# Kernel tuning notes

Hardware: AMD Instinct MI355X
Metric: run time of the kernel (lower is better)

The kernel has to match this reference:

```python
import jax, jax.numpy as jnp
import numpy as np

D_MODEL = 512
EXPAND = 2
D_INNER = D_MODEL * EXPAND  # 1024
D_STATE = 64
D_CONV = 4
DT_BASE = 0.1
MAX_STEPS = 10
THRESH = 1e-4
DAMPING = 0.5
B_SZ, L = 1, 256


def setup_inputs() -> dict:
    key = jax.random.key(0)
    ks = jax.random.split(key, 12)
    rn = lambda k, shape, s=0.02: jax.random.normal(k, shape, jnp.float32) * s
    x = jax.random.normal(ks[0], (B_SZ, L, D_MODEL), jnp.float32)
    # in_proj: Linear(d_model -> 2*d_inner, bias=False); stored (in, out)
    W_in = rn(ks[1], (D_MODEL, 2 * D_INNER))
    # depthwise causal conv1d, kernel (d_inner, 1, d_conv) + bias
    conv_w = rn(ks[2], (D_INNER, 1, D_CONV), 0.2)
    conv_b = rn(ks[3], (D_INNER,), 0.02)
    # SSM kernel params (A_log initialized exactly as in the module)
    A_log = jnp.log(jnp.broadcast_to(jnp.arange(1, D_STATE + 1, dtype=jnp.float32), (D_INNER, D_STATE)))
    W_B = rn(ks[4], (D_INNER, D_STATE))
    W_C = rn(ks[5], (D_INNER, D_STATE))
    D = jnp.ones((D_INNER,), jnp.float32)
    dt_w1 = rn(ks[6], (D_INNER, D_INNER // 4))
    dt_b1 = jnp.zeros((D_INNER // 4,), jnp.float32)
    dt_w2 = rn(ks[7], (D_INNER // 4, D_INNER))
    dt_b2 = jnp.zeros((D_INNER,), jnp.float32)
    W_out = rn(ks[8], (D_INNER, D_MODEL))
    ln_in_g = jnp.ones((D_MODEL,), jnp.float32)
    ln_in_b = jnp.zeros((D_MODEL,), jnp.float32)
    ln_out_g = jnp.ones((D_MODEL,), jnp.float32)
    ln_out_b = jnp.zeros((D_MODEL,), jnp.float32)
    return dict(x=x, W_in=W_in, conv_w=conv_w, conv_b=conv_b, A_log=A_log, W_B=W_B, W_C=W_C, D=D,
                dt_w1=dt_w1, dt_b1=dt_b1, dt_w2=dt_w2, dt_b2=dt_b2, W_out=W_out,
                ln_in_g=ln_in_g, ln_in_b=ln_in_b, ln_out_g=ln_out_g, ln_out_b=ln_out_b)


def _ln(x, g, b, eps=1e-5):
    m = jnp.mean(x, axis=-1, keepdims=True)
    v = jnp.mean((x - m) ** 2, axis=-1, keepdims=True)
    return (x - m) / jnp.sqrt(v + eps) * g + b


def _forward(x, W_in, conv_w, conv_b, A_log, W_B, W_C, D, dt_w1, dt_b1, dt_w2, dt_b2, W_out,
             ln_in_g, ln_in_b, ln_out_g, ln_out_b):
    residual = x
    xn = _ln(x, ln_in_g, ln_in_b)
    xz = xn @ W_in                                  # (b, l, 2*d_inner)
    x_inner, z = jnp.split(xz, 2, axis=-1)
    # depthwise causal conv (pad d_conv-1 on the left == pad both sides then take [:L])
    xc = jnp.transpose(x_inner, (0, 2, 1))          # (b, d, l)
    xc = jax.lax.conv_general_dilated(xc, conv_w, window_strides=(1,),
                                      padding=[(D_CONV - 1, 0)],
                                      feature_group_count=D_INNER)
    xc = xc + conv_b[None, :, None]
    x_inner = jax.nn.silu(jnp.transpose(xc, (0, 2, 1)))  # (b, l, d_inner)

    # --- kernel quantities (loop-invariant: depend only on x_inner) ---
    A = -jnp.exp(A_log)                             # (d, n)
    Bm = x_inner @ W_B                              # (b, l, n)
    Cm = x_inner @ W_C                              # (b, l, n)
    dt = jax.nn.gelu(x_inner @ dt_w1 + dt_b1, approximate=False) @ dt_w2 + dt_b2
    dt = jax.nn.softplus(dt) * DT_BASE              # (b, l, d)
    A_bar = jnp.exp(jnp.einsum('bld,dn->bldn', dt, A))          # (b, l, d, n)
    Bx = (dt * x_inner)[..., None] * Bm[:, :, None, :]           # B_bar * x, (b, l, d, n)

    # --- fixed-point evolution with convergence-gated freeze (== early break) ---
    h = jnp.zeros_like(A_bar)
    y_h = h  # h_new that produces the output y
    converged = jnp.array(False)
    h_diff = jnp.float32(0.0)
    for _ in range(MAX_STEPS):
        h_new = A_bar * h + Bx
        dh = h_new - h
        diff = jnp.mean(jnp.sqrt(jnp.sum(dh * dh, axis=(-2, -1))))  # mean Frobenius norm over (b,l)
        y_h = jnp.where(converged, y_h, h_new)
        h_diff = jnp.where(converged, h_diff, diff)
        converged = converged | (diff < THRESH)
        # damping update skipped after break (converged)
        h = jnp.where(converged, h, DAMPING * h_new + (1.0 - DAMPING) * h)

    y = jnp.einsum('bldn,bln->bld', y_h, Cm) + D * x_inner
    y = y * jax.nn.silu(z)
    out = _ln(y @ W_out, ln_out_g, ln_out_b) + residual
    return out


def reference(x, W_in, conv_w, conv_b, A_log, W_B, W_C, D, dt_w1, dt_b1, dt_w2, dt_b2, W_out,
              ln_in_g, ln_in_b, ln_out_g, ln_out_b):
    return _forward(x, W_in, conv_w, conv_b, A_log, W_B, W_C, D, dt_w1, dt_b1, dt_w2, dt_b2,
                    W_out, ln_in_g, ln_in_b, ln_out_g, ln_out_b)
```

## Files before the change

kernel.cpp:

```cpp
#include <hip/hip_runtime.h>
#include <cmath>

#define L 256
#define DMODEL 512
#define DINNER 1024
#define DSTATE 64
#define NSTEPS 10
#define TK 32

template <int NS>
__global__ __launch_bounds__(256) void ln_kernel(
    const float* __restrict__ in, int islice, const float* __restrict__ g,
    const float* __restrict__ b, const float* __restrict__ resid,
    float* __restrict__ out) {
  const int l = blockIdx.x, tid = threadIdx.x;
  float x0 = 0.0f, x1 = 0.0f;
#pragma unroll
  for (int s = 0; s < NS; ++s) {
    x0 += in[s * islice + l * DMODEL + tid];
    x1 += in[s * islice + l * DMODEL + tid + 256];
  }
  float sm = x0 + x1, q = x0 * x0 + x1 * x1;
#pragma unroll
  for (int off = 32; off; off >>= 1) {
    sm += __shfl_down(sm, off);
    q += __shfl_down(q, off);
  }
  __shared__ float sw[4], qw[4];
  __shared__ float mS, rS;
  if ((tid & 63) == 0) { sw[tid >> 6] = sm; qw[tid >> 6] = q; }
  __syncthreads();
  if (tid == 0) {
    float S = sw[0] + sw[1] + sw[2] + sw[3];
    float Q = qw[0] + qw[1] + qw[2] + qw[3];
    float m = S * (1.0f / DMODEL);
    float v = Q * (1.0f / DMODEL) - m * m;
    mS = m;
    rS = rsqrtf(v + 1e-5f);
  }
  __syncthreads();
  const float m = mS, r = rS;
  float o0 = (x0 - m) * r * g[tid] + b[tid];
  float o1 = (x1 - m) * r * g[tid + 256] + b[tid + 256];
  if (resid) {
    o0 += resid[l * DMODEL + tid];
    o1 += resid[l * DMODEL + tid + 256];
  }
  out[l * DMODEL + tid] = o0;
  out[l * DMODEL + tid + 256] = o1;
}

template <int MODE>
__global__ __launch_bounds__(256) void gemm32(
    const float* __restrict__ A, int lda, int aslice,
    const float* __restrict__ B, int ldb, float* __restrict__ C, int ldc,
    int cslice, int kchunk, const float* __restrict__ abias,
    const float* __restrict__ WB, const float* __restrict__ WC,
    const float* __restrict__ W1) {
  __shared__ float As[TK][33];
  __shared__ float Bs[TK][64];
  const int tid = threadIdx.x;
  const int tx = tid & 15, ty = tid >> 4;
  const int m0 = blockIdx.y * 32, n0 = blockIdx.x * 64;
  const int k0 = blockIdx.z * kchunk;
  const float* Bp = B;
  int ld = ldb, nb = n0;
  if (MODE == 1) {
    if (n0 < 64) { Bp = WB; ld = 64; nb = n0; }
    else if (n0 < 128) { Bp = WC; ld = 64; nb = n0 - 64; }
    else { Bp = W1; ld = 256; nb = n0 - 128; }
  }
  const int ar = tid >> 3, ac = (tid & 7) * 4;
  const int br = tid >> 4, bc = (tid & 15) * 4;
  float acc[2][4] = {};
  for (int kk0 = 0; kk0 < kchunk; kk0 += TK) {
    const int kb = k0 + kk0;
    float v[4];
    if (MODE == 2) {
      v[0] = v[1] = v[2] = v[3] = 0.0f;
#pragma unroll
      for (int s = 0; s < 4; ++s) {
        const float4 t =
            *(const float4*)&A[s * aslice + (m0 + ar) * lda + kb + ac];
        v[0] += t.x; v[1] += t.y; v[2] += t.z; v[3] += t.w;
      }
#pragma unroll
      for (int j = 0; j < 4; ++j) {
        const float x = v[j] + abias[kb + ac + j];
        v[j] = 0.5f * x * (1.0f + erff(x * 0.70710678118654752f));
      }
    } else {
      const float4 t = *(const float4*)&A[(m0 + ar) * lda + kb + ac];
      v[0] = t.x; v[1] = t.y; v[2] = t.z; v[3] = t.w;
    }
#pragma unroll
    for (int j = 0; j < 4; ++j) As[ac + j][ar] = v[j];
#pragma unroll
    for (int i = 0; i < 2; ++i)
      *(float4*)&Bs[br + i * 16][bc] =
          *(const float4*)&Bp[(kb + br + i * 16) * ld + nb + bc];
    __syncthreads();
#pragma unroll
    for (int kk = 0; kk < TK; ++kk) {
      const float a0 = As[kk][ty * 2], a1 = As[kk][ty * 2 + 1];
      const float4 bv = *(const float4*)&Bs[kk][tx * 4];
      const float* bp = (const float*)&bv;
#pragma unroll
      for (int j = 0; j < 4; ++j) {
        acc[0][j] = fmaf(a0, bp[j], acc[0][j]);
        acc[1][j] = fmaf(a1, bp[j], acc[1][j]);
      }
    }
    __syncthreads();
  }
  float* Cp = C + (size_t)blockIdx.z * cslice;
#pragma unroll
  for (int i = 0; i < 2; ++i)
    *(float4*)&Cp[(m0 + ty * 2 + i) * ldc + n0 + tx * 4] = *(float4*)&acc[i][0];
}

__global__ __launch_bounds__(256) void conv_silu_kernel(
    const float* __restrict__ xz, const float* __restrict__ cw,
    const float* __restrict__ cb, float* __restrict__ xi) {
  const int d = blockIdx.x * 256 + threadIdx.x;
  const int l = blockIdx.y;
  const float4 w = *(const float4*)&cw[d * 4];
  const float* wp = (const float*)&w;
  float s = cb[d];
#pragma unroll
  for (int j = 0; j < 4; ++j) {
    const int ll = l - 3 + j;
    if (ll >= 0) s = fmaf(wp[j], xz[ll * (2 * DINNER) + d], s);
  }
  xi[l * DINNER + d] = s / (1.0f + expf(-s));
}

__global__ __launch_bounds__(256) void pass1_kernel(
    const float* __restrict__ dtbp, const float* __restrict__ dt_b2,
    const float* __restrict__ xi, const float* __restrict__ bctp,
    float* __restrict__ accLp) {
  const int l = blockIdx.y, tid = threadIdx.x;
  const int d = blockIdx.x * 256 + tid;
  __shared__ float B2[DSTATE];
  if (tid < DSTATE) {
    float b = 0.0f;
#pragma unroll
    for (int s = 0; s < 4; ++s) b += bctp[s * 98304 + l * 384 + tid];
    B2[tid] = b * b;
  }
  __syncthreads();
  const float dr =
      dtbp[l * DINNER + d] + dtbp[262144 + l * DINNER + d] + dt_b2[d];
  const float sp = (dr > 20.0f) ? dr : log1pf(expf(dr));
  const float dtv = 0.1f * sp;
  const float xv = xi[l * DINNER + d];
  float w0 = dtv * xv;
  w0 *= w0;
  const float q = expf(-dtv);
  float acc[NSTEPS] = {};
  float a = 1.0f;
  for (int n = 0; n < DSTATE; ++n) {
    a *= q;
    const float r = fmaf(0.5f, a, 0.5f);
    const float s2 = r * r;
    float p = w0 * B2[n];
#pragma unroll
    for (int k = 0; k < NSTEPS; ++k) {
      acc[k] += p;
      p *= s2;
    }
  }
  __shared__ float sred[4][NSTEPS];
#pragma unroll
  for (int k = 0; k < NSTEPS; ++k) {
    float v = acc[k];
#pragma unroll
    for (int off = 32; off; off >>= 1) v += __shfl_down(v, off);
    if ((tid & 63) == 0) sred[tid >> 6][k] = v;
  }
  __syncthreads();
  if (tid < NSTEPS)
    accLp[blockIdx.x * (L * NSTEPS) + l * NSTEPS + tid] =
        sred[0][tid] + sred[1][tid] + sred[2][tid] + sred[3][tid];
}

__global__ __launch_bounds__(256) void pass2_kernel(
    const float* __restrict__ dtbp, const float* __restrict__ dt_b2,
    const float* __restrict__ xi, const float* __restrict__ bctp,
    const float* __restrict__ xz, const float* __restrict__ Dv,
    const float* __restrict__ accLp, float* __restrict__ y) {
  const int l = blockIdx.y, tid = threadIdx.x;
  const int d = blockIdx.x * 256 + tid;
  __shared__ float sred[4];
  __shared__ float diffs[NSTEPS];
  __shared__ int Ksh;
#pragma unroll
  for (int k = 0; k < NSTEPS; ++k) {
    float v = accLp[tid * NSTEPS + k] + accLp[2560 + tid * NSTEPS + k] +
              accLp[5120 + tid * NSTEPS + k] + accLp[7680 + tid * NSTEPS + k];
    v = sqrtf(v);
#pragma unroll
    for (int off = 32; off; off >>= 1) v += __shfl_down(v, off);
    if ((tid & 63) == 0) sred[tid >> 6] = v;
    __syncthreads();
    if (tid == 0)
      diffs[k] = (sred[0] + sred[1] + sred[2] + sred[3]) * (1.0f / L);
    __syncthreads();
  }
  __shared__ float P[DSTATE];
  if (tid == 0) {
    int K = NSTEPS;
    for (int k = 0; k < NSTEPS; ++k) {
      if (diffs[k] < 1e-4f) { K = k + 1; break; }
    }
    Ksh = K;
  }
  if (tid < DSTATE) {
    float bm = 0.0f, cm = 0.0f;
#pragma unroll
    for (int s = 0; s < 4; ++s) {
      bm += bctp[s * 98304 + l * 384 + tid];
      cm += bctp[s * 98304 + l * 384 + 64 + tid];
    }
    P[tid] = bm * cm;
  }
  __syncthreads();
  const int K = Ksh;
  const float dr =
      dtbp[l * DINNER + d] + dtbp[262144 + l * DINNER + d] + dt_b2[d];
  const float sp = (dr > 20.0f) ? dr : log1pf(expf(dr));
  const float dtv = 0.1f * sp;
  const float xv = xi[l * DINNER + d];
  const float dtx = dtv * xv;
  const float q = expf(-dtv);
  float a = 1.0f, s = 0.0f;
  for (int n = 0; n < DSTATE; ++n) {
    a *= q;
    const float r = fmaf(0.5f, a, 0.5f);
    float c = 0.0f;
    for (int k = 1; k < K; ++k) c = fmaf(r, c, 0.5f);
    const float hn = fmaf(a, c, 1.0f);
    s = fmaf(hn, P[n], s);
  }
  float yv = fmaf(dtx, s, Dv[d] * xv);
  const float zv = xz[l * (2 * DINNER) + DINNER + d];
  yv *= zv / (1.0f + expf(-zv));
  y[l * DINNER + d] = yv;
}

extern "C" void kernel_launch(void* const* d_in, const int* in_sizes, int n_in,
                              void* d_out, int out_size, void* d_ws,
                              size_t ws_size, hipStream_t stream) {
  const float* x = (const float*)d_in[0];
  const float* W_in = (const float*)d_in[1];
  const float* conv_w = (const float*)d_in[2];
  const float* conv_b = (const float*)d_in[3];
  const float* W_B = (const float*)d_in[5];
  const float* W_C = (const float*)d_in[6];
  const float* Dv = (const float*)d_in[7];
  const float* dt_w1 = (const float*)d_in[8];
  const float* dt_b1 = (const float*)d_in[9];
  const float* dt_w2 = (const float*)d_in[10];
  const float* dt_b2 = (const float*)d_in[11];
  const float* W_out = (const float*)d_in[12];
  const float* ln_in_g = (const float*)d_in[13];
  const float* ln_in_b = (const float*)d_in[14];
  const float* ln_out_g = (const float*)d_in[15];
  const float* ln_out_b = (const float*)d_in[16];
  float* out = (float*)d_out;

  float* ws = (float*)d_ws;
  float* xn = ws;
  float* xz = xn + 131072;
  float* xi = xz + 524288;
  float* bctp = xi + 262144;
  float* dtbp = bctp + 393216;
  float* accLp = dtbp + 524288;
  float* yop = accLp + 10240;

  ln_kernel<1><<<L, 256, 0, stream>>>(x, 0, ln_in_g, ln_in_b, nullptr, xn);
  gemm32<0><<<dim3(32, 8, 1), 256, 0, stream>>>(
      xn, DMODEL, 0, W_in, 2 * DINNER, xz, 2 * DINNER, 0, DMODEL, nullptr,
      nullptr, nullptr, nullptr);
  conv_silu_kernel<<<dim3(4, L), 256, 0, stream>>>(xz, conv_w, conv_b, xi);
  gemm32<1><<<dim3(6, 8, 4), 256, 0, stream>>>(
      xi, DINNER, 0, nullptr, 0, bctp, 384, 98304, 256, nullptr, W_B, W_C,
      dt_w1);
  gemm32<2><<<dim3(16, 8, 2), 256, 0, stream>>>(
      bctp + 128, 384, 98304, dt_w2, DINNER, dtbp, DINNER, 262144, 128, dt_b1,
      nullptr, nullptr, nullptr);
  pass1_kernel<<<dim3(4, L), 256, 0, stream>>>(dtbp, dt_b2, xi, bctp, accLp);
  pass2_kernel<<<dim3(4, L), 256, 0, stream>>>(dtbp, dt_b2, xi, bctp, xz, Dv,
                                               accLp, xi);
  gemm32<0><<<dim3(8, 8, 4), 256, 0, stream>>>(
      xi, DINNER, 0, W_out, DMODEL, yop, DMODEL, 131072, 256, nullptr, nullptr,
      nullptr, nullptr);
  ln_kernel<4><<<L, 256, 0, stream>>>(yop, 131072, ln_out_g, ln_out_b, x, out);
}
```

Baseline: 192.3 us.

## Fuse all stages into one cooperative persistent kernel with grid syncs

Replaces the nine separate kernel launches with a single cooperative kernel of 512 blocks that runs each stage in turn, separated by grid-wide barriers. Work splits are changed so every stage uses about 512 blocks: more split-K partials, two channels per thread in the elementwise passes, and a separate single-block K-selection stage. The goal is to remove launch gaps and tail effects between many small stages. In exchange it adds grid-sync cost, writes more partial buffers that readers must sum, and keeps a multi-launch fallback if the cooperative launch fails.

```diff
diff --git a/kernel.cpp b/kernel.cpp
--- a/kernel.cpp
+++ b/kernel.cpp
@@ -1,45 +1,70 @@
 #include <hip/hip_runtime.h>
+#include <hip/hip_cooperative_groups.h>
 #include <cmath>
+
+namespace cg = cooperative_groups;
 
 #define L 256
 #define DMODEL 512
 #define DINNER 1024
 #define DSTATE 64
 #define NSTEPS 10
-#define TK 32
+
+struct Args {
+  const float *x, *W_in, *conv_w, *conv_b, *W_B, *W_C, *Dv;
+  const float *dt_w1, *dt_b1, *dt_w2, *dt_b2, *W_out;
+  const float *ln_in_g, *ln_in_b, *ln_out_g, *ln_out_b;
+  float* out;
+  float *xn, *xz, *xi, *bctp, *dtbp, *accLp, *yop;
+  int* Kp;
+};
+
+struct SMem {
+  float As[32][34];
+  float Bs[32][64];
+  float red[4][NSTEPS];
+  float vec[DSTATE];
+  float diffs[NSTEPS];
+  float mS, rS;
+};
+
+__device__ __forceinline__ float gelu_f(float x) {
+  return 0.5f * x * (1.0f + erff(x * 0.70710678118654752f));
+}
 
 template <int NS>
-__global__ __launch_bounds__(256) void ln_kernel(
-    const float* __restrict__ in, int islice, const float* __restrict__ g,
-    const float* __restrict__ b, const float* __restrict__ resid,
-    float* __restrict__ out) {
-  const int l = blockIdx.x, tid = threadIdx.x;
+__device__ void stage_ln(SMem& sm, const float* in, int islice, const float* g,
+                         const float* b, const float* resid, float* out,
+                         int gid, int tid) {
+  if (gid >= 256) return;
+  const int l = gid;
   float x0 = 0.0f, x1 = 0.0f;
 #pragma unroll
   for (int s = 0; s < NS; ++s) {
     x0 += in[s * islice + l * DMODEL + tid];
     x1 += in[s * islice + l * DMODEL + tid + 256];
   }
-  float sm = x0 + x1, q = x0 * x0 + x1 * x1;
+  float sv = x0 + x1, q = x0 * x0 + x1 * x1;
 #pragma unroll
   for (int off = 32; off; off >>= 1) {
-    sm += __shfl_down(sm, off);
+    sv += __shfl_down(sv, off);
     q += __shfl_down(q, off);
   }
-  __shared__ float sw[4], qw[4];
-  __shared__ float mS, rS;
-  if ((tid & 63) == 0) { sw[tid >> 6] = sm; qw[tid >> 6] = q; }
+  if ((tid & 63) == 0) {
+    sm.red[tid >> 6][0] = sv;
+    sm.red[tid >> 6][1] = q;
+  }
   __syncthreads();
   if (tid == 0) {
-    float S = sw[0] + sw[1] + sw[2] + sw[3];
-    float Q = qw[0] + qw[1] + qw[2] + qw[3];
+    float S = sm.red[0][0] + sm.red[1][0] + sm.red[2][0] + sm.red[3][0];
+    float Q = sm.red[0][1] + sm.red[1][1] + sm.red[2][1] + sm.red[3][1];
     float m = S * (1.0f / DMODEL);
     float v = Q * (1.0f / DMODEL) - m * m;
-    mS = m;
-    rS = rsqrtf(v + 1e-5f);
-  }
-  __syncthreads();
-  const float m = mS, r = rS;
+    sm.mS = m;
+    sm.rS = rsqrtf(v + 1e-5f);
+  }
+  __syncthreads();
+  const float m = sm.mS, r = sm.rS;
   float o0 = (x0 - m) * r * g[tid] + b[tid];
   float o1 = (x1 - m) * r * g[tid + 256] + b[tid + 256];
   if (resid) {
@@ -50,250 +75,321 @@
   out[l * DMODEL + tid + 256] = o1;
 }
 
-template <int MODE>
-__global__ __launch_bounds__(256) void gemm32(
-    const float* __restrict__ A, int lda, int aslice,
-    const float* __restrict__ B, int ldb, float* __restrict__ C, int ldc,
-    int cslice, int kchunk, const float* __restrict__ abias,
-    const float* __restrict__ WB, const float* __restrict__ WC,
-    const float* __restrict__ W1) {
-  __shared__ float As[TK][33];
-  __shared__ float Bs[TK][64];
-  const int tid = threadIdx.x;
-  const int tx = tid & 15, ty = tid >> 4;
-  const int m0 = blockIdx.y * 32, n0 = blockIdx.x * 64;
-  const int k0 = blockIdx.z * kchunk;
-  const float* Bp = B;
-  int ld = ldb, nb = n0;
-  if (MODE == 1) {
-    if (n0 < 64) { Bp = WB; ld = 64; nb = n0; }
-    else if (n0 < 128) { Bp = WC; ld = 64; nb = n0 - 64; }
-    else { Bp = W1; ld = 256; nb = n0 - 128; }
-  }
-  const int ar = tid >> 3, ac = (tid & 7) * 4;
+__device__ void gemm_tile(SMem& sm, const float* A, int lda, int aslice,
+                          int nslA, const float* abias, const float* B, int ldb,
+                          int nb, float* C, int ldc, int nc, int m0, int kbase,
+                          int ktiles, int tid) {
+  const int rowg = tid >> 4, colg = tid & 15;
+  float acc0[4] = {}, acc1[4] = {};
+  const int ar = tid >> 3, ka = (tid & 7) * 4;
   const int br = tid >> 4, bc = (tid & 15) * 4;
-  float acc[2][4] = {};
-  for (int kk0 = 0; kk0 < kchunk; kk0 += TK) {
-    const int kb = k0 + kk0;
-    float v[4];
-    if (MODE == 2) {
-      v[0] = v[1] = v[2] = v[3] = 0.0f;
-#pragma unroll
-      for (int s = 0; s < 4; ++s) {
-        const float4 t =
-            *(const float4*)&A[s * aslice + (m0 + ar) * lda + kb + ac];
-        v[0] += t.x; v[1] += t.y; v[2] += t.z; v[3] += t.w;
+  for (int t = 0; t < ktiles; ++t) {
+    const int kb = kbase + t * 32;
+    {
+      const float* ap = &A[(size_t)(m0 + ar) * lda + kb + ka];
+      float v[4];
+      if (nslA == 1) {
+        const float4 t4 = *(const float4*)ap;
+        v[0] = t4.x; v[1] = t4.y; v[2] = t4.z; v[3] = t4.w;
+      } else {
+        v[0] = v[1] = v[2] = v[3] = 0.0f;
+        for (int s = 0; s < nslA; ++s) {
+          const float4 t4 = *(const float4*)&ap[(size_t)s * aslice];
+          v[0] += t4.x; v[1] += t4.y; v[2] += t4.z; v[3] += t4.w;
+        }
       }
+      if (abias) {
+#pragma unroll
+        for (int j = 0; j < 4; ++j) v[j] = gelu_f(v[j] + abias[kb + ka + j]);
+      }
+#pragma unroll
+      for (int j = 0; j < 4; ++j) sm.As[ka + j][ar] = v[j];
+    }
+#pragma unroll
+    for (int i = 0; i < 2; ++i)
+      *(float4*)&sm.Bs[br + 16 * i][bc] =
+          *(const float4*)&B[(size_t)(kb + br + 16 * i) * ldb + nb + bc];
+    __syncthreads();
+#pragma unroll
+    for (int kk = 0; kk < 32; ++kk) {
+      const float2 av = *(const float2*)&sm.As[kk][rowg * 2];
+      const float4 bv = *(const float4*)&sm.Bs[kk][colg * 4];
+      const float* bp = (const float*)&bv;
 #pragma unroll
       for (int j = 0; j < 4; ++j) {
-        const float x = v[j] + abias[kb + ac + j];
-        v[j] = 0.5f * x * (1.0f + erff(x * 0.70710678118654752f));
+        acc0[j] = fmaf(av.x, bp[j], acc0[j]);
+        acc1[j] = fmaf(av.y, bp[j], acc1[j]);
       }
-    } else {
-      const float4 t = *(const float4*)&A[(m0 + ar) * lda + kb + ac];
-      v[0] = t.x; v[1] = t.y; v[2] = t.z; v[3] = t.w;
-    }
-#pragma unroll
-    for (int j = 0; j < 4; ++j) As[ac + j][ar] = v[j];
-#pragma unroll
-    for (int i = 0; i < 2; ++i)
-      *(float4*)&Bs[br + i * 16][bc] =
-          *(const float4*)&Bp[(kb + br + i * 16) * ld + nb + bc];
+    }
     __syncthreads();
-#pragma unroll
-    for (int kk = 0; kk < TK; ++kk) {
-      const float a0 = As[kk][ty * 2], a1 = As[kk][ty * 2 + 1];
-      const float4 bv = *(const float4*)&Bs[kk][tx * 4];
-      const float* bp = (const float*)&bv;
-#pragma unroll
-      for (int j = 0; j < 4; ++j) {
-        acc[0][j] = fmaf(a0, bp[j], acc[0][j]);
-        acc[1][j] = fmaf(a1, bp[j], acc[1][j]);
-      }
-    }
-    __syncthreads();
-  }
-  float* Cp = C + (size_t)blockIdx.z * cslice;
-#pragma unroll
-  for (int i = 0; i < 2; ++i)
-    *(float4*)&Cp[(m0 + ty * 2 + i) * ldc + n0 + tx * 4] = *(float4*)&acc[i][0];
-}
-
-__global__ __launch_bounds__(256) void conv_silu_kernel(
-    const float* __restrict__ xz, const float* __restrict__ cw,
-    const float* __restrict__ cb, float* __restrict__ xi) {
-  const int d = blockIdx.x * 256 + threadIdx.x;
-  const int l = blockIdx.y;
-  const float4 w = *(const float4*)&cw[d * 4];
-  const float* wp = (const float*)&w;
-  float s = cb[d];
-#pragma unroll
-  for (int j = 0; j < 4; ++j) {
-    const int ll = l - 3 + j;
-    if (ll >= 0) s = fmaf(wp[j], xz[ll * (2 * DINNER) + d], s);
-  }
-  xi[l * DINNER + d] = s / (1.0f + expf(-s));
-}
-
-__global__ __launch_bounds__(256) void pass1_kernel(
-    const float* __restrict__ dtbp, const float* __restrict__ dt_b2,
-    const float* __restrict__ xi, const float* __restrict__ bctp,
-    float* __restrict__ accLp) {
-  const int l = blockIdx.y, tid = threadIdx.x;
-  const int d = blockIdx.x * 256 + tid;
-  __shared__ float B2[DSTATE];
+  }
+  *(float4*)&C[(size_t)(m0 + rowg * 2) * ldc + nc + colg * 4] =
+      *(float4*)&acc0[0];
+  *(float4*)&C[(size_t)(m0 + rowg * 2 + 1) * ldc + nc + colg * 4] =
+      *(float4*)&acc1[0];
+}
+
+__device__ void stage_inproj(const Args& a, SMem& sm, int gid, int tid) {
+  if (gid >= 512) return;
+  const int kz = gid >> 8, rem = gid & 255;
+  const int mt = rem >> 5, nt = rem & 31;
+  gemm_tile(sm, a.xn, DMODEL, 0, 1, nullptr, a.W_in, 2048, nt * 64,
+            a.xz + kz * 524288, 2048, nt * 64, mt * 32, kz * 256, 8, tid);
+}
+
+__device__ void stage_conv(const Args& a, int gid, int tid) {
+  if (gid >= 512) return;
+  const int l = gid >> 1;
+#pragma unroll
+  for (int dd = 0; dd < 2; ++dd) {
+    const int d = (gid & 1) * 512 + dd * 256 + tid;
+    const float4 w = *(const float4*)&a.conv_w[d * 4];
+    const float* wp = (const float*)&w;
+    float s = a.conv_b[d];
+#pragma unroll
+    for (int j = 0; j < 4; ++j) {
+      const int ll = l - 3 + j;
+      if (ll >= 0)
+        s = fmaf(wp[j], a.xz[ll * 2048 + d] + a.xz[524288 + ll * 2048 + d], s);
+    }
+    a.xi[l * DINNER + d] = s / (1.0f + expf(-s));
+  }
+}
+
+__device__ void stage_bct(const Args& a, SMem& sm, int gid, int tid) {
+  if (gid >= 384) return;
+  const int kz = gid / 48, rem = gid % 48;
+  const int mt = rem / 6, nt = rem % 6;
+  const float* Bp;
+  int ldb, nb;
+  if (nt == 0) { Bp = a.W_B; ldb = 64; nb = 0; }
+  else if (nt == 1) { Bp = a.W_C; ldb = 64; nb = 0; }
+  else { Bp = a.dt_w1; ldb = 256; nb = (nt - 2) * 64; }
+  gemm_tile(sm, a.xi, DINNER, 0, 1, nullptr, Bp, ldb, nb, a.bctp + kz * 98304,
+            384, nt * 64, mt * 32, kz * 128, 4, tid);
+}
+
+__device__ void stage_dt2(const Args& a, SMem& sm, int gid, int tid) {
+  if (gid >= 512) return;
+  const int kz = gid >> 7, rem = gid & 127;
+  const int mt = rem >> 4, nt = rem & 15;
+  gemm_tile(sm, a.bctp + 128, 384, 98304, 8, a.dt_b1, a.dt_w2, 1024, nt * 64,
+            a.dtbp + kz * 262144, 1024, nt * 64, mt * 32, kz * 64, 2, tid);
+}
+
+__device__ void stage_pass1(const Args& a, SMem& sm, int gid, int tid) {
+  if (gid >= 512) return;
+  const int l = gid >> 1, bx = gid & 1;
   if (tid < DSTATE) {
     float b = 0.0f;
 #pragma unroll
-    for (int s = 0; s < 4; ++s) b += bctp[s * 98304 + l * 384 + tid];
-    B2[tid] = b * b;
-  }
-  __syncthreads();
-  const float dr =
-      dtbp[l * DINNER + d] + dtbp[262144 + l * DINNER + d] + dt_b2[d];
-  const float sp = (dr > 20.0f) ? dr : log1pf(expf(dr));
-  const float dtv = 0.1f * sp;
-  const float xv = xi[l * DINNER + d];
-  float w0 = dtv * xv;
-  w0 *= w0;
-  const float q = expf(-dtv);
+    for (int s = 0; s < 8; ++s) b += a.bctp[s * 98304 + l * 384 + tid];
+    sm.vec[tid] = b * b;
+  }
+  __syncthreads();
   float acc[NSTEPS] = {};
-  float a = 1.0f;
-  for (int n = 0; n < DSTATE; ++n) {
-    a *= q;
-    const float r = fmaf(0.5f, a, 0.5f);
-    const float s2 = r * r;
-    float p = w0 * B2[n];
-#pragma unroll
-    for (int k = 0; k < NSTEPS; ++k) {
-      acc[k] += p;
-      p *= s2;
-    }
-  }
-  __shared__ float sred[4][NSTEPS];
+#pragma unroll
+  for (int dd = 0; dd < 2; ++dd) {
+    const int d = bx * 512 + dd * 256 + tid;
+    float dr = a.dt_b2[d];
+#pragma unroll
+    for (int s = 0; s < 4; ++s) dr += a.dtbp[s * 262144 + l * DINNER + d];
+    const float sp = (dr > 20.0f) ? dr : log1pf(expf(dr));
+    const float dtv = 0.1f * sp;
+    const float xv = a.xi[l * DINNER + d];
+    float w0 = dtv * xv;
+    w0 *= w0;
+    const float q = expf(-dtv);
+    float aa = 1.0f;
+    for (int n = 0; n < DSTATE; ++n) {
+      aa *= q;
+      const float r = fmaf(0.5f, aa, 0.5f);
+      const float s2 = r * r;
+      float p = w0 * sm.vec[n];
+#pragma unroll
+      for (int k = 0; k < NSTEPS; ++k) {
+        acc[k] += p;
+        p *= s2;
+      }
+    }
+  }
 #pragma unroll
   for (int k = 0; k < NSTEPS; ++k) {
     float v = acc[k];
 #pragma unroll
     for (int off = 32; off; off >>= 1) v += __shfl_down(v, off);
-    if ((tid & 63) == 0) sred[tid >> 6][k] = v;
+    if ((tid & 63) == 0) sm.red[tid >> 6][k] = v;
   }
   __syncthreads();
   if (tid < NSTEPS)
-    accLp[blockIdx.x * (L * NSTEPS) + l * NSTEPS + tid] =
-        sred[0][tid] + sred[1][tid] + sred[2][tid] + sred[3][tid];
-}
-
-__global__ __launch_bounds__(256) void pass2_kernel(
-    const float* __restrict__ dtbp, const float* __restrict__ dt_b2,
-    const float* __restrict__ xi, const float* __restrict__ bctp,
-    const float* __restrict__ xz, const float* __restrict__ Dv,
-    const float* __restrict__ accLp, float* __restrict__ y) {
-  const int l = blockIdx.y, tid = threadIdx.x;
-  const int d = blockIdx.x * 256 + tid;
-  __shared__ float sred[4];
-  __shared__ float diffs[NSTEPS];
-  __shared__ int Ksh;
+    a.accLp[bx * 2560 + l * NSTEPS + tid] =
+        sm.red[0][tid] + sm.red[1][tid] + sm.red[2][tid] + sm.red[3][tid];
+}
+
+__device__ void stage_kselect(const Args& a, SMem& sm, int gid, int tid) {
+  if (gid != 0) return;
 #pragma unroll
   for (int k = 0; k < NSTEPS; ++k) {
-    float v = accLp[tid * NSTEPS + k] + accLp[2560 + tid * NSTEPS + k] +
-              accLp[5120 + tid * NSTEPS + k] + accLp[7680 + tid * NSTEPS + k];
+    float v = a.accLp[tid * NSTEPS + k] + a.accLp[2560 + tid * NSTEPS + k];
     v = sqrtf(v);
 #pragma unroll
     for (int off = 32; off; off >>= 1) v += __shfl_down(v, off);
-    if ((tid & 63) == 0) sred[tid >> 6] = v;
+    if ((tid & 63) == 0) sm.red[tid >> 6][0] = v;
     __syncthreads();
     if (tid == 0)
-      diffs[k] = (sred[0] + sred[1] + sred[2] + sred[3]) * (1.0f / L);
+      sm.diffs[k] = (sm.red[0][0] + sm.red[1][0] + sm.red[2][0] + sm.red[3][0]) *
+                    (1.0f / L);
     __syncthreads();
   }
-  __shared__ float P[DSTATE];
   if (tid == 0) {
     int K = NSTEPS;
     for (int k = 0; k < NSTEPS; ++k) {
-      if (diffs[k] < 1e-4f) { K = k + 1; break; }
-    }
-    Ksh = K;
-  }
+      if (sm.diffs[k] < 1e-4f) { K = k + 1; break; }
+    }
+    a.Kp[0] = K;
+  }
+}
+
+__device__ void stage_pass2(const Args& a, SMem& sm, int gid, int tid) {
+  if (gid >= 512) return;
+  const int l = gid >> 1, bx = gid & 1;
   if (tid < DSTATE) {
     float bm = 0.0f, cm = 0.0f;
 #pragma unroll
-    for (int s = 0; s < 4; ++s) {
-      bm += bctp[s * 98304 + l * 384 + tid];
-      cm += bctp[s * 98304 + l * 384 + 64 + tid];
-    }
-    P[tid] = bm * cm;
-  }
-  __syncthreads();
-  const int K = Ksh;
-  const float dr =
-      dtbp[l * DINNER + d] + dtbp[262144 + l * DINNER + d] + dt_b2[d];
-  const float sp = (dr > 20.0f) ? dr : log1pf(expf(dr));
-  const float dtv = 0.1f * sp;
-  const float xv = xi[l * DINNER + d];
-  const float dtx = dtv * xv;
-  const float q = expf(-dtv);
-  float a = 1.0f, s = 0.0f;
-  for (int n = 0; n < DSTATE; ++n) {
-    a *= q;
-    const float r = fmaf(0.5f, a, 0.5f);
-    float c = 0.0f;
-    for (int k = 1; k < K; ++k) c = fmaf(r, c, 0.5f);
-    const float hn = fmaf(a, c, 1.0f);
-    s = fmaf(hn, P[n], s);
-  }
-  float yv = fmaf(dtx, s, Dv[d] * xv);
-  const float zv = xz[l * (2 * DINNER) + DINNER + d];
-  yv *= zv / (1.0f + expf(-zv));
-  y[l * DINNER + d] = yv;
+    for (int s = 0; s < 8; ++s) {
+      bm += a.bctp[s * 98304 + l * 384 + tid];
+      cm += a.bctp[s * 98304 + l * 384 + 64 + tid];
+    }
+    sm.vec[tid] = bm * cm;
+  }
+  __syncthreads();
+  const int K = a.Kp[0];
+#pragma unroll
+  for (int dd = 0; dd < 2; ++dd) {
+    const int d = bx * 512 + dd * 256 + tid;
+    float dr = a.dt_b2[d];
+#pragma unroll
+    for (int s = 0; s < 4; ++s) dr += a.dtbp[s * 262144 + l * DINNER + d];
+    const float sp = (dr > 20.0f) ? dr : log1pf(expf(dr));
+    const float dtv = 0.1f * sp;
+    const float xv = a.xi[l * DINNER + d];
+    const float dtx = dtv * xv;
+    const float q = expf(-dtv);
+    float aa = 1.0f, s = 0.0f;
+    for (int n = 0; n < DSTATE; ++n) {
+      aa *= q;
+      const float r = fmaf(0.5f, aa, 0.5f);
+      float c = 0.0f;
+      for (int k = 1; k < K; ++k) c = fmaf(r, c, 0.5f);
+      const float hn = fmaf(aa, c, 1.0f);
+      s = fmaf(hn, sm.vec[n], s);
+    }
+    float yv = fmaf(dtx, s, a.Dv[d] * xv);
+    const float zv =
+        a.xz[l * 2048 + 1024 + d] + a.xz[524288 + l * 2048 + 1024 + d];
+    yv *= zv / (1.0f + expf(-zv));
+    a.xi[l * DINNER + d] = yv;
+  }
+}
+
+__device__ void stage_outproj(const Args& a, SMem& sm, int gid, int tid) {
+  if (gid >= 512) return;
+  const int kz = gid >> 6, rem = gid & 63;
+  const int mt = rem >> 3, nt = rem & 7;
+  gemm_tile(sm, a.xi, DINNER, 0, 1, nullptr, a.W_out, DMODEL, nt * 64,
+            a.yop + kz * 131072, DMODEL, nt * 64, mt * 32, kz * 128, 4, tid);
+}
+
+__global__ __launch_bounds__(256, 2) void fused_kernel(Args a) {
+  __shared__ SMem sm;
+  cg::grid_group grid = cg::this_grid();
+  const int gid = blockIdx.x, tid = threadIdx.x;
+  stage_ln<1>(sm, a.x, 0, a.ln_in_g, a.ln_in_b, nullptr, a.xn, gid, tid);
+  grid.sync();
+  stage_inproj(a, sm, gid, tid);
+  grid.sync();
+  stage_conv(a, gid, tid);
+  grid.sync();
+  stage_bct(a, sm, gid, tid);
+  grid.sync();
+  stage_dt2(a, sm, gid, tid);
+  grid.sync();
+  stage_pass1(a, sm, gid, tid);
+  grid.sync();
+  stage_kselect(a, sm, gid, tid);
+  grid.sync();
+  stage_pass2(a, sm, gid, tid);
+  grid.sync();
+  stage_outproj(a, sm, gid, tid);
+  grid.sync();
+  stage_ln<8>(sm, a.yop, 131072, a.ln_out_g, a.ln_out_b, a.x, a.out, gid, tid);
+}
+
+template <int S>
+__global__ __launch_bounds__(256, 2) void stage_kernel(Args a) {
+  __shared__ SMem sm;
+  const int gid = blockIdx.x, tid = threadIdx.x;
+  if constexpr (S == 0)
+    stage_ln<1>(sm, a.x, 0, a.ln_in_g, a.ln_in_b, nullptr, a.xn, gid, tid);
+  else if constexpr (S == 1) stage_inproj(a, sm, gid, tid);
+  else if constexpr (S == 2) stage_conv(a, gid, tid);
+  else if constexpr (S == 3) stage_bct(a, sm, gid, tid);
+  else if constexpr (S == 4) stage_dt2(a, sm, gid, tid);
+  else if constexpr (S == 5) stage_pass1(a, sm, gid, tid);
+  else if constexpr (S == 6) stage_kselect(a, sm, gid, tid);
+  else if constexpr (S == 7) stage_pass2(a, sm, gid, tid);
+  else if constexpr (S == 8) stage_outproj(a, sm, gid, tid);
+  else if constexpr (S == 9)
+    stage_ln<8>(sm, a.yop, 131072, a.ln_out_g, a.ln_out_b, a.x, a.out, gid,
+                tid);
 }
 
 extern "C" void kernel_launch(void* const* d_in, const int* in_sizes, int n_in,
                               void* d_out, int out_size, void* d_ws,
                               size_t ws_size, hipStream_t stream) {
-  const float* x = (const float*)d_in[0];
-  const float* W_in = (const float*)d_in[1];
-  const float* conv_w = (const float*)d_in[2];
-  const float* conv_b = (const float*)d_in[3];
-  const float* W_B = (const float*)d_in[5];
-  const float* W_C = (const float*)d_in[6];
-  const float* Dv = (const float*)d_in[7];
-  const float* dt_w1 = (const float*)d_in[8];
-  const float* dt_b1 = (const float*)d_in[9];
-  const float* dt_w2 = (const float*)d_in[10];
-  const float* dt_b2 = (const float*)d_in[11];
-  const float* W_out = (const float*)d_in[12];
-  const float* ln_in_g = (const float*)d_in[13];
-  const float* ln_in_b = (const float*)d_in[14];
-  const float* ln_out_g = (const float*)d_in[15];
-  const float* ln_out_b = (const float*)d_in[16];
-  float* out = (float*)d_out;
+  Args a;
+  a.x = (const float*)d_in[0];
+  a.W_in = (const float*)d_in[1];
+  a.conv_w = (const float*)d_in[2];
+  a.conv_b = (const float*)d_in[3];
+  a.W_B = (const float*)d_in[5];
+  a.W_C = (const float*)d_in[6];
+  a.Dv = (const float*)d_in[7];
+  a.dt_w1 = (const float*)d_in[8];
+  a.dt_b1 = (const float*)d_in[9];
+  a.dt_w2 = (const float*)d_in[10];
+  a.dt_b2 = (const float*)d_in[11];
+  a.W_out = (const float*)d_in[12];
+  a.ln_in_g = (const float*)d_in[13];
+  a.ln_in_b = (const float*)d_in[14];
+  a.ln_out_g = (const float*)d_in[15];
+  a.ln_out_b = (const float*)d_in[16];
+  a.out = (float*)d_out;
 
   float* ws = (float*)d_ws;
-  float* xn = ws;
-  float* xz = xn + 131072;
-  float* xi = xz + 524288;
-  float* bctp = xi + 262144;
-  float* dtbp = bctp + 393216;
-  float* accLp = dtbp + 524288;
-  float* yop = accLp + 10240;
-
-  ln_kernel<1><<<L, 256, 0, stream>>>(x, 0, ln_in_g, ln_in_b, nullptr, xn);
-  gemm32<0><<<dim3(32, 8, 1), 256, 0, stream>>>(
-      xn, DMODEL, 0, W_in, 2 * DINNER, xz, 2 * DINNER, 0, DMODEL, nullptr,
-      nullptr, nullptr, nullptr);
-  conv_silu_kernel<<<dim3(4, L), 256, 0, stream>>>(xz, conv_w, conv_b, xi);
-  gemm32<1><<<dim3(6, 8, 4), 256, 0, stream>>>(
-      xi, DINNER, 0, nullptr, 0, bctp, 384, 98304, 256, nullptr, W_B, W_C,
-      dt_w1);
-  gemm32<2><<<dim3(16, 8, 2), 256, 0, stream>>>(
-      bctp + 128, 384, 98304, dt_w2, DINNER, dtbp, DINNER, 262144, 128, dt_b1,
-      nullptr, nullptr, nullptr);
-  pass1_kernel<<<dim3(4, L), 256, 0, stream>>>(dtbp, dt_b2, xi, bctp, accLp);
-  pass2_kernel<<<dim3(4, L), 256, 0, stream>>>(dtbp, dt_b2, xi, bctp, xz, Dv,
-                                               accLp, xi);
-  gemm32<0><<<dim3(8, 8, 4), 256, 0, stream>>>(
-      xi, DINNER, 0, W_out, DMODEL, yop, DMODEL, 131072, 256, nullptr, nullptr,
-      nullptr, nullptr);
-  ln_kernel<4><<<L, 256, 0, stream>>>(yop, 131072, ln_out_g, ln_out_b, x, out);
-}
+  a.xn = ws;
+  a.xz = a.xn + 131072;
+  a.xi = a.xz + 1048576;
+  a.bctp = a.xi + 262144;
+  a.dtbp = a.bctp + 786432;
+  a.accLp = a.dtbp + 1048576;
+  a.yop = a.accLp + 5120;
+  a.Kp = (int*)(a.yop + 1048576);
+
+  void* kargs[] = {&a};
+  hipError_t e = hipLaunchCooperativeKernel((const void*)fused_kernel,
+                                            dim3(512), dim3(256), kargs, 0,
+                                            stream);
+  if (e != hipSuccess) {
+    stage_kernel<0><<<256, 256, 0, stream>>>(a);
+    stage_kernel<1><<<512, 256, 0, stream>>>(a);
+    stage_kernel<2><<<512, 256, 0, stream>>>(a);
+    stage_kernel<3><<<384, 256, 0, stream>>>(a);
+    stage_kernel<4><<<512, 256, 0, stream>>>(a);
+    stage_kernel<5><<<512, 256, 0, stream>>>(a);
+    stage_kernel<6><<<1, 256, 0, stream>>>(a);
+    stage_kernel<7><<<512, 256, 0, stream>>>(a);
+    stage_kernel<8><<<512, 256, 0, stream>>>(a);
+    stage_kernel<9><<<256, 256, 0, stream>>>(a);
+  }
+}
```

After: 682.7 us. 255% more time.
